# Kernel tuning notes

Hardware: AMD Instinct MI355X
Metric: run time of the kernel (lower is better)

Reference implementation:

```python
import jax, jax.numpy as jnp
import numpy as np

B, N, E, D = 8, 10000, 160000, 256
H = D // 2
SLOPE = 0.2  # LeakyReLU negative slope


def setup_inputs() -> dict:
    key = jax.random.key(0)
    ks = jax.random.split(key, 8)
    node_feats = jax.random.normal(ks[0], (B, N, D), dtype=jnp.float32)
    edge_attr = jax.random.uniform(ks[1], (E, 1), dtype=jnp.float32)
    W1 = jax.random.normal(ks[2], (2 * D, H), dtype=jnp.float32) * 0.05
    b1 = jnp.zeros((H,), dtype=jnp.float32)
    W2 = jax.random.normal(ks[3], (H, 1), dtype=jnp.float32) * 0.05
    b2 = jnp.zeros((1,), dtype=jnp.float32)
    edge_index = jax.random.randint(ks[4], (2, E), 0, N, dtype=jnp.int64)
    valid_masks = jax.random.randint(ks[5], (B, N), 0, 2).astype(bool)
    return {"node_feats": node_feats, "edge_attr": edge_attr, "W1": W1, "b1": b1,
            "W2": W2, "b2": b2, "edge_index": edge_index, "valid_masks": valid_masks}


def reference(node_feats, edge_attr, W1, b1, W2, b2, edge_index, valid_masks):
    # node_feats: [B,N,D]; edge_index: [2,E] shared across batch
    d = node_feats.shape[-1]
    src, dst = edge_index[0], edge_index[1]
    # cat([src_feats, dst_feats]) @ W1 == src @ W1[:d] + dst @ W1[d:]
    # Project per-node first, then gather per-edge: avoids the [B,E,2D] concat.
    ps = jnp.einsum('bnd,dh->bnh', node_feats, W1[:d])   # [B,N,H]
    pd = jnp.einsum('bnd,dh->bnh', node_feats, W1[d:])   # [B,N,H]
    h = ps[:, src] + pd[:, dst] + b1                      # [B,E,H]
    h = jnp.where(h >= 0, h, SLOPE * h)                   # LeakyReLU(0.2)
    scores = jnp.einsum('beh,h->be', h, W2[:, 0]) + b2[0]  # [B,E]
    scores = scores * edge_attr[:, 0]                     # edge_attr multiplies pre-softmax
    w = jax.nn.softmax(scores, axis=1)                    # global softmax over all edges
    # sparse_coo(edge_index, w) @ node_feats: out[src[e]] += w[e] * feats[dst[e]]
    msg = w[..., None] * node_feats[:, dst]               # [B,E,D]
    n = node_feats.shape[1]
    agg = jax.vmap(lambda m: jax.ops.segment_sum(m, src, num_segments=n))(msg)  # [B,N,D]
    mask = valid_masks.astype(node_feats.dtype)           # [B,N]
    cnt = mask.sum(axis=1)                                # [B]
    masked_mean = (agg * mask[..., None]).sum(axis=1) / jnp.maximum(cnt, 1.0)[:, None]
    full_mean = agg.mean(axis=1)
    graph_feats = jnp.where((cnt > 0)[:, None], masked_mean, full_mean)  # [B,D]
    return graph_feats, w
```

## Files before the change

### kernel.cpp

```cpp
#include <hip/hip_runtime.h>
#include <hip/hip_bf16.h>
#include <hip/hip_fp16.h>

#define B_ 8
#define N_ 10000
#define E_ 160000
#define D_ 256
#define H_ 128
#define SLOPE 0.2f
#define NCHUNK 50

#define EC_ 16
#define NR_ 32
#define RANGE_ 320
#define NPAD_ (NR_ * RANGE_)

typedef __attribute__((ext_vector_type(8))) _Float16 v8h;
typedef __attribute__((ext_vector_type(4))) _Float16 v4h;
typedef __attribute__((ext_vector_type(4))) float f32x4;

__global__ __launch_bounds__(64) void k_detect(const int* __restrict__ eidx_raw,
                                               const unsigned int* __restrict__ mask32,
                                               int* __restrict__ flags) {
    const int t = threadIdx.x;
    unsigned long long oddnz = __ballot(eidx_raw[2 * t + 1] != 0);
    unsigned long long mgt1  = __ballot(mask32[t] > 1u);
    if (t == 0) {
        flags[0] = (oddnz == 0ull) ? 1 : 0;
        flags[1] = (mgt1 != 0ull) ? 1 : 0;
    }
}

__global__ __launch_bounds__(256) void k_canon(const int* __restrict__ eidx_raw,
                                               const unsigned char* __restrict__ mask8,
                                               const unsigned int* __restrict__ mask32,
                                               const int* __restrict__ flags,
                                               int* __restrict__ ce,
                                               unsigned char* __restrict__ cm,
                                               unsigned char* __restrict__ cmT) {
    const int i = blockIdx.x * 256 + threadIdx.x;
    const int f_e = flags[0], f_m = flags[1];
    if (i < 2 * E_) ce[i] = f_e ? eidx_raw[2 * i] : eidx_raw[i];
    if (i < B_ * N_) {
        unsigned char v = f_m ? (unsigned char)(mask8[i] != 0)
                              : (unsigned char)(mask32[i] != 0u);
        cm[i] = v;
        const int b = i / N_;
        const int n = i - b * N_;
        cmT[n * 8 + b] = v;
    }
}

__global__ __launch_bounds__(256) void kW(const float* __restrict__ W1,
                                          __half* __restrict__ Wt) {
    const int i = blockIdx.x * 256 + threadIdx.x;
    const int f = i & 127;
    const int row = i >> 7;
    const int c = row >> 8, k = row & 255;
    Wt[((c * 128 + f) * 256) + k] = __float2half(W1[row * 128 + f]);
}

__global__ __launch_bounds__(256) void k0_init(const unsigned char* __restrict__ cm,
                                               float* __restrict__ cnt) {
    const int b = blockIdx.x;
    const int tid = threadIdx.x;
    int c = 0;
    for (int i = tid; i < N_; i += 256) c += cm[b * N_ + i] ? 1 : 0;
    __shared__ int red[256];
    red[tid] = c;
    __syncthreads();
    for (int s = 128; s > 0; s >>= 1) {
        if (tid < s) red[tid] += red[tid + s];
        __syncthreads();
    }
    if (tid == 0) cnt[b] = (float)red[0];
}

__global__ __launch_bounds__(256) void k1_mfma(const float* __restrict__ X,
                                               const __half* __restrict__ Wt,
                                               __half* __restrict__ ps,
                                               __half* __restrict__ pd) {
    const int cb = blockIdx.y;
    const int rb = blockIdx.x;
    const int tid = threadIdx.x;
    const int wave = tid >> 6, lane = tid & 63;
    const int quad = lane >> 4, l16 = lane & 15;

    __shared__ _Float16 Xs[128 * 40];
    __shared__ _Float16 Ws[128 * 40];

    f32x4 acc[2][8];
#pragma unroll
    for (int i = 0; i < 2; i++)
#pragma unroll
        for (int j = 0; j < 8; j++) acc[i][j] = (f32x4){0.f, 0.f, 0.f, 0.f};

    const int row_base = rb * 128;
    const __half* __restrict__ Wh = Wt + (size_t)cb * 128 * 256;
    __half* __restrict__ outp = cb ? pd : ps;

    const int sr = tid >> 1;
    const int sh = tid & 1;

    for (int kc = 0; kc < 8; ++kc) {
        {
            const float4* src = (const float4*)&X[(size_t)(row_base + sr) * 256 + kc * 32 + sh * 16];
            _Float16* dst = &Xs[sr * 40 + sh * 16];
#pragma unroll
            for (int j = 0; j < 4; ++j) {
                float4 v = src[j];
                v4h p = {(_Float16)v.x, (_Float16)v.y, (_Float16)v.z, (_Float16)v.w};
                *(v4h*)&dst[j * 4] = p;
            }
        }
        {
            const float4* src = (const float4*)&Wh[(size_t)sr * 256 + kc * 32 + sh * 16];
            float4 v0 = src[0], v1 = src[1];
            *(float4*)&Ws[sr * 40 + sh * 16] = v0;
            *(float4*)&Ws[sr * 40 + sh * 16 + 8] = v1;
        }
        __syncthreads();

        v8h wf[2];
#pragma unroll
        for (int ft = 0; ft < 2; ++ft)
            wf[ft] = *(v8h*)&Ws[(wave * 32 + ft * 16 + l16) * 40 + quad * 8];
#pragma unroll
        for (int nt = 0; nt < 8; ++nt) {
            v8h xf = *(v8h*)&Xs[(nt * 16 + l16) * 40 + quad * 8];
            acc[0][nt] = __builtin_amdgcn_mfma_f32_16x16x32_f16(wf[0], xf, acc[0][nt], 0, 0, 0);
            acc[1][nt] = __builtin_amdgcn_mfma_f32_16x16x32_f16(wf[1], xf, acc[1][nt], 0, 0, 0);
        }
        __syncthreads();
    }

#pragma unroll
    for (int nt = 0; nt < 8; ++nt) {
        const int R = row_base + nt * 16 + l16;
        const int b = R / N_;
        const int n = R - b * N_;
        __half* base = outp + ((size_t)(n * 8 + b)) * 128 + wave * 32 + quad * 4;
#pragma unroll
        for (int ft = 0; ft < 2; ++ft) {
            f32x4 a = acc[ft][nt];
            v4h h = {(_Float16)a.x, (_Float16)a.y, (_Float16)a.z, (_Float16)a.w};
            *(v4h*)(base + ft * 16) = h;
        }
    }
}

__global__ __launch_bounds__(256) void k2_scores(const __half* __restrict__ ps,
                                                 const __half* __restrict__ pd,
                                                 const int* __restrict__ ce,
                                                 const float* __restrict__ b1,
                                                 const float* __restrict__ W2,
                                                 const float* __restrict__ b2,
                                                 const float* __restrict__ eattr,
                                                 float* __restrict__ scores) {
    __shared__ float sb1[128];
    __shared__ float sw2[128];
    const int tid = threadIdx.x;
    if (tid < 128) sb1[tid] = b1[tid];
    else sw2[tid - 128] = W2[tid - 128];
    __syncthreads();

    const int wave = tid >> 6;
    const int lane = tid & 63;
    const int e = blockIdx.x * 4 + wave;

    const int src = ce[e];
    const int dst = ce[E_ + e];
    const int b = lane >> 3;
    const int hi = (lane & 7) * 16;

    const float4* pps = (const float4*)&ps[((size_t)src * 8 + b) * 128 + hi];
    const float4* ppd = (const float4*)&pd[((size_t)dst * 8 + b) * 128 + hi];

    float partial = 0.f;
#pragma unroll
    for (int q = 0; q < 2; q++) {
        float4 rs = pps[q];
        float4 rd = ppd[q];
        const __half2* hs = (const __half2*)&rs;
        const __half2* hd = (const __half2*)&rd;
#pragma unroll
        for (int j = 0; j < 4; j++) {
            float2 fs = __half22float2(hs[j]);
            float2 fd = __half22float2(hd[j]);
            int idx = hi + q * 8 + j * 2;
            float h0 = fs.x + fd.x + sb1[idx];     h0 = h0 >= 0.f ? h0 : SLOPE * h0;
            float h1 = fs.y + fd.y + sb1[idx + 1]; h1 = h1 >= 0.f ? h1 : SLOPE * h1;
            partial = fmaf(h0, sw2[idx], partial);
            partial = fmaf(h1, sw2[idx + 1], partial);
        }
    }
    partial += __shfl_xor(partial, 1);
    partial += __shfl_xor(partial, 2);
    partial += __shfl_xor(partial, 4);

    if ((lane & 7) == 0) {
        scores[(size_t)b * E_ + e] = (partial + b2[0]) * eattr[e];
    }
}

__global__ __launch_bounds__(256) void k3a_max(const float* __restrict__ sc,
                                               float* __restrict__ pmax) {
    const int b = blockIdx.y, c = blockIdx.x, tid = threadIdx.x;
    const float* x = sc + (size_t)b * E_;
    const int i0 = c * (E_ / 32);
    float mv = -3.4e38f;
    for (int i = i0 + tid; i < i0 + E_ / 32; i += 256) mv = fmaxf(mv, x[i]);
    __shared__ float red[256];
    red[tid] = mv;
    __syncthreads();
    for (int s = 128; s > 0; s >>= 1) {
        if (tid < s) red[tid] = fmaxf(red[tid], red[tid + s]);
        __syncthreads();
    }
    if (tid == 0) pmax[b * 32 + c] = red[0];
}

__global__ __launch_bounds__(256) void k3b_maxred(const float* __restrict__ pmax,
                                                  float* __restrict__ m) {
    const int t = threadIdx.x;
    float v = pmax[t];
#pragma unroll
    for (int k = 1; k <= 16; k <<= 1) v = fmaxf(v, __shfl_xor(v, k));
    if ((t & 31) == 0) m[t >> 5] = v;
}

__global__ __launch_bounds__(256) void k3c_sum(const float* __restrict__ sc,
                                               const float* __restrict__ m,
                                               double* __restrict__ psum) {
    const int b = blockIdx.y, c = blockIdx.x, tid = threadIdx.x;
    const float* x = sc + (size_t)b * E_;
    const float mv = m[b];
    const int i0 = c * (E_ / 32);
    double s = 0.0;
    for (int i = i0 + tid; i < i0 + E_ / 32; i += 256) s += (double)expf(x[i] - mv);
    __shared__ double red[256];
    red[tid] = s;
    __syncthreads();
    for (int st = 128; st > 0; st >>= 1) {
        if (tid < st) red[tid] += red[tid + st];
        __syncthreads();
    }
    if (tid == 0) psum[b * 32 + c] = red[0];
}

__global__ __launch_bounds__(256) void k3d_sumred(const double* __restrict__ psum,
                                                  float* __restrict__ inv) {
    const int t = threadIdx.x;
    double v = psum[t];
#pragma unroll
    for (int k = 1; k <= 16; k <<= 1) v += __shfl_xor(v, k);
    if ((t & 31) == 0) inv[t >> 5] = (float)(1.0 / v);
}

__global__ __launch_bounds__(256) void k3e_norm(float* __restrict__ sc,
                                                const float* __restrict__ m,
                                                const float* __restrict__ inv,
                                                float* __restrict__ wT) {
    const int e = blockIdx.x * 256 + threadIdx.x;
    float wv[8];
#pragma unroll
    for (int b = 0; b < 8; b++) {
        float v = expf(sc[(size_t)b * E_ + e] - m[b]) * inv[b];
        sc[(size_t)b * E_ + e] = v;
        wv[b] = v;
    }
    *(float4*)&wT[(size_t)e * 8]     = make_float4(wv[0], wv[1], wv[2], wv[3]);
    *(float4*)&wT[(size_t)e * 8 + 4] = make_float4(wv[4], wv[5], wv[6], wv[7]);
}

__global__ __launch_bounds__(256) void k3f_bin(const int* __restrict__ ce,
                                               const float* __restrict__ wT,
                                               const unsigned char* __restrict__ cmT,
                                               float* __restrict__ Wpart) {
    const int ec = blockIdx.x;
    const int rg = blockIdx.y;
    const int n0 = rg * RANGE_;

    __shared__ float lWf[RANGE_ * 8];
    __shared__ float lWm[RANGE_ * 8];
    for (int i = threadIdx.x; i < RANGE_ * 8; i += 256) { lWf[i] = 0.f; lWm[i] = 0.f; }
    __syncthreads();

    const int4* dst4 = (const int4*)(ce + E_);
    const int base4 = ec * (E_ / EC_ / 4);
    for (int i = threadIdx.x; i < E_ / EC_ / 4; i += 256) {
        int4 d4 = dst4[base4 + i];
        int dd[4] = {d4.x, d4.y, d4.z, d4.w};
        const int e0 = (base4 + i) * 4;
#pragma unroll
        for (int j = 0; j < 4; ++j) {
            const int rel = dd[j] - n0;
            if ((unsigned)rel < (unsigned)RANGE_) {
                const int e = e0 + j;
                const int src = ce[e];
                float4 w0 = *(const float4*)&wT[(size_t)e * 8];
                float4 w1 = *(const float4*)&wT[(size_t)e * 8 + 4];
                const unsigned long long mm = *(const unsigned long long*)&cmT[src * 8];
                float wv[8] = {w0.x, w0.y, w0.z, w0.w, w1.x, w1.y, w1.z, w1.w};
                float* lf = &lWf[rel * 8];
                float* lm = &lWm[rel * 8];
#pragma unroll
                for (int b = 0; b < 8; b++) {
                    atomicAdd(&lf[b], wv[b]);
                    if ((mm >> (8 * b)) & 1ull) atomicAdd(&lm[b], wv[b]);
                }
            }
        }
    }
    __syncthreads();

    float* of = Wpart + ((size_t)ec * 2 + 0) * (NPAD_ * 8) + n0 * 8;
    float* om = Wpart + ((size_t)ec * 2 + 1) * (NPAD_ * 8) + n0 * 8;
    for (int i = threadIdx.x; i < RANGE_ * 8; i += 256) { of[i] = lWf[i]; om[i] = lWm[i]; }
}

__global__ __launch_bounds__(256) void k3g_reduce(const float* __restrict__ Wpart,
                                                  float* __restrict__ WfT,
                                                  float* __restrict__ WmT) {
    const int i = blockIdx.x * 256 + threadIdx.x;
    float sf = 0.f, sm = 0.f;
#pragma unroll
    for (int ec = 0; ec < EC_; ec++) {
        sf += Wpart[(size_t)ec * 2 * (NPAD_ * 8) + i];
        sm += Wpart[((size_t)ec * 2 + 1) * (NPAD_ * 8) + i];
    }
    WfT[i] = sf;
    WmT[i] = sm;
}

__global__ __launch_bounds__(256) void k4b_wsum(const float* __restrict__ X,
                                                const float* __restrict__ WmT,
                                                const float* __restrict__ WfT,
                                                float* __restrict__ gpart) {
    const int c = blockIdx.x;
    const int b = blockIdx.y;
    const int tx = threadIdx.x & 63;
    const int ty = threadIdx.x >> 6;
    const int npc = N_ / NCHUNK;
    const int n0 = c * npc;

    const float4* X4 = (const float4*)(X + (size_t)b * N_ * 256);
    float4 am = {0.f, 0.f, 0.f, 0.f};
    float4 af = {0.f, 0.f, 0.f, 0.f};

    for (int n = n0 + ty; n < n0 + npc; n += 4) {
        float wm = WmT[n * 8 + b];
        float wf = WfT[n * 8 + b];
        float4 v = X4[(size_t)n * 64 + tx];
        am.x = fmaf(wm, v.x, am.x); am.y = fmaf(wm, v.y, am.y);
        am.z = fmaf(wm, v.z, am.z); am.w = fmaf(wm, v.w, am.w);
        af.x = fmaf(wf, v.x, af.x); af.y = fmaf(wf, v.y, af.y);
        af.z = fmaf(wf, v.z, af.z); af.w = fmaf(wf, v.w, af.w);
    }

    __shared__ float4 red[256];
    red[threadIdx.x] = am;
    __syncthreads();
    if (ty == 0) {
        float4 r1 = red[tx + 64], r2 = red[tx + 128], r3 = red[tx + 192];
        am.x += r1.x + r2.x + r3.x; am.y += r1.y + r2.y + r3.y;
        am.z += r1.z + r2.z + r3.z; am.w += r1.w + r2.w + r3.w;
    }
    __syncthreads();
    red[threadIdx.x] = af;
    __syncthreads();
    if (ty == 0) {
        float4 r1 = red[tx + 64], r2 = red[tx + 128], r3 = red[tx + 192];
        af.x += r1.x + r2.x + r3.x; af.y += r1.y + r2.y + r3.y;
        af.z += r1.z + r2.z + r3.z; af.w += r1.w + r2.w + r3.w;
        float4* gp4 = (float4*)gpart;
        gp4[((c * 2 + 0) * 8 + b) * 64 + tx] = am;
        gp4[((c * 2 + 1) * 8 + b) * 64 + tx] = af;
    }
}

__global__ __launch_bounds__(256) void k5_final(const float* __restrict__ gpart,
                                                const float* __restrict__ cnt,
                                                float* __restrict__ gf) {
    const int b = blockIdx.x;
    const int d = threadIdx.x;
    float sm = 0.f, sf = 0.f;
    for (int c = 0; c < NCHUNK; c++) {
        sm += gpart[((c * 2 + 0) * 8 + b) * 256 + d];
        sf += gpart[((c * 2 + 1) * 8 + b) * 256 + d];
    }
    const float cn = cnt[b];
    gf[b * 256 + d] = (cn > 0.f) ? (sm / cn) : (sf / (float)N_);
}

extern "C" void kernel_launch(void* const* d_in, const int* in_sizes, int n_in,
                              void* d_out, int out_size, void* d_ws, size_t ws_size,
                              hipStream_t stream) {
    const float* X     = (const float*)d_in[0];
    const float* eattr = (const float*)d_in[1];
    const float* W1    = (const float*)d_in[2];
    const float* b1    = (const float*)d_in[3];
    const float* W2    = (const float*)d_in[4];
    const float* b2    = (const float*)d_in[5];
    const int*   eidx_raw = (const int*)d_in[6];
    const unsigned char* mask8 = (const unsigned char*)d_in[7];
    const unsigned int*  mask32 = (const unsigned int*)d_in[7];

    float* out  = (float*)d_out;
    float* gf   = out;
    float* wout = out + 2048;

    __half* ps_h = (__half*)d_ws;
    __half* pd_h = ps_h + (size_t)N_ * 8 * 128;
    __half* Wt   = pd_h + (size_t)N_ * 8 * 128;
    int* ce = (int*)(Wt + 2 * 128 * 256);
    unsigned char* cmT = (unsigned char*)(ce + 2 * E_);
    unsigned char* cm  = cmT + NPAD_ * 8;
    float* cnt = (float*)(cm + B_ * N_);
    int* flags = (int*)(cnt + 8);
    float* pmax = (float*)(flags + 2);
    float* mbuf = pmax + 256;
    float* invb = mbuf + 8;
    double* psum = (double*)(((uintptr_t)(invb + 8) + 15) & ~(uintptr_t)15);
    float* gpart = (float*)(psum + 256);

    float* wT    = (float*)d_ws;
    float* Wpart = wT + (size_t)E_ * 8;
    float* WfT   = Wpart + (size_t)EC_ * 2 * NPAD_ * 8;
    float* WmT   = WfT + NPAD_ * 8;

    hipLaunchKernelGGL(k_detect, dim3(1), dim3(64), 0, stream, eidx_raw, mask32, flags);
    hipLaunchKernelGGL(k_canon, dim3(1250), dim3(256), 0, stream,
                       eidx_raw, mask8, mask32, flags, ce, cm, cmT);
    hipLaunchKernelGGL(kW, dim3(256), dim3(256), 0, stream, W1, Wt);
    hipLaunchKernelGGL(k0_init, dim3(8), dim3(256), 0, stream, cm, cnt);
    hipLaunchKernelGGL(k1_mfma, dim3(625, 2), dim3(256), 0, stream, X, Wt, ps_h, pd_h);
    hipLaunchKernelGGL(k2_scores, dim3(E_ / 4), dim3(256), 0, stream,
                       ps_h, pd_h, ce, b1, W2, b2, eattr, wout);
    hipLaunchKernelGGL(k3a_max, dim3(32, 8), dim3(256), 0, stream, wout, pmax);
    hipLaunchKernelGGL(k3b_maxred, dim3(1), dim3(256), 0, stream, pmax, mbuf);
    hipLaunchKernelGGL(k3c_sum, dim3(32, 8), dim3(256), 0, stream, wout, mbuf, psum);
    hipLaunchKernelGGL(k3d_sumred, dim3(1), dim3(256), 0, stream, psum, invb);
    hipLaunchKernelGGL(k3e_norm, dim3(E_ / 256), dim3(256), 0, stream,
                       wout, mbuf, invb, wT);
    hipLaunchKernelGGL(k3f_bin, dim3(EC_, NR_), dim3(256), 0, stream, ce, wT, cmT, Wpart);
    hipLaunchKernelGGL(k3g_reduce, dim3(NPAD_ * 8 / 256), dim3(256), 0, stream,
                       Wpart, WfT, WmT);
    hipLaunchKernelGGL(k4b_wsum, dim3(NCHUNK, 8), dim3(256), 0, stream, X, WmT, WfT, gpart);
    hipLaunchKernelGGL(k5_final, dim3(8), dim3(256), 0, stream, gpart, cnt, gf);
}
```

Measured before the change: 326.0 us.

## Bin-sort edges by src/dst node ranges and use packed fp16 dot2 scoring

Adds a histogram, prefix and scatter pass that reorders edges into 16x16 bins by destination and source node range. The score kernel then walks edges in this order, with an XCD-aware block remap, so gathers of ps/pd rows hit cache better. It also computes LeakyReLU and the W2 dot product in packed half precision using fdot2, with b1 and W2 pre-converted to fp16. The cost is three extra small kernels, indirect score writes through the original edge index, and lower precision in the score accumulation inputs.

```diff
diff --git a/kernel.cpp b/kernel.cpp
--- a/kernel.cpp
+++ b/kernel.cpp
@@ -15,9 +15,23 @@
 #define RANGE_ 320
 #define NPAD_ (NR_ * RANGE_)
 
+#define NB_ 64
+#define EPB_ (E_ / NB_)
+#define BINS_ 256
+#define NPB_ (N_ / 16)
+
 typedef __attribute__((ext_vector_type(8))) _Float16 v8h;
 typedef __attribute__((ext_vector_type(4))) _Float16 v4h;
+typedef __attribute__((ext_vector_type(2))) _Float16 v2h;
 typedef __attribute__((ext_vector_type(4))) float f32x4;
+
+static __device__ __forceinline__ float dot2f(v2h a, v2h b, float c) {
+#if __has_builtin(__builtin_amdgcn_fdot2)
+    return __builtin_amdgcn_fdot2(a, b, c, false);
+#else
+    return fmaf((float)a.y, (float)b.y, fmaf((float)a.x, (float)b.x, c));
+#endif
+}
 
 __global__ __launch_bounds__(64) void k_detect(const int* __restrict__ eidx_raw,
                                                const unsigned int* __restrict__ mask32,
@@ -52,12 +66,20 @@
 }
 
 __global__ __launch_bounds__(256) void kW(const float* __restrict__ W1,
-                                          __half* __restrict__ Wt) {
+                                          const float* __restrict__ b1,
+                                          const float* __restrict__ W2,
+                                          __half* __restrict__ Wt,
+                                          __half* __restrict__ b1h,
+                                          __half* __restrict__ w2h) {
     const int i = blockIdx.x * 256 + threadIdx.x;
     const int f = i & 127;
     const int row = i >> 7;
     const int c = row >> 8, k = row & 255;
     Wt[((c * 128 + f) * 256) + k] = __float2half(W1[row * 128 + f]);
+    if (blockIdx.x == 0 && threadIdx.x < 128) {
+        b1h[threadIdx.x] = __float2half(b1[threadIdx.x]);
+        w2h[threadIdx.x] = __float2half(W2[threadIdx.x]);
+    }
 }
 
 __global__ __launch_bounds__(256) void k0_init(const unsigned char* __restrict__ cm,
@@ -74,6 +96,64 @@
         __syncthreads();
     }
     if (tid == 0) cnt[b] = (float)red[0];
+}
+
+__global__ __launch_bounds__(256) void khist(const int* __restrict__ ce,
+                                             int* __restrict__ hpart) {
+    __shared__ int h[BINS_];
+    const int tid = threadIdx.x;
+    h[tid] = 0;
+    __syncthreads();
+    const int base = blockIdx.x * EPB_;
+    for (int i = tid; i < EPB_; i += 256) {
+        const int s = ce[base + i], d = ce[E_ + base + i];
+        const int bin = (d / NPB_) * 16 + s / NPB_;
+        atomicAdd(&h[bin], 1);
+    }
+    __syncthreads();
+    hpart[blockIdx.x * BINS_ + tid] = h[tid];
+}
+
+__global__ __launch_bounds__(256) void kprefix(const int* __restrict__ hpart,
+                                               int* __restrict__ offsetG) {
+    __shared__ int cnt[BINS_];
+    __shared__ int excl[BINS_];
+    const int bin = threadIdx.x;
+    int c = 0;
+    for (int b = 0; b < NB_; b++) c += hpart[b * BINS_ + bin];
+    cnt[bin] = c;
+    __syncthreads();
+    if (bin == 0) {
+        int r = 0;
+        for (int i = 0; i < BINS_; i++) { excl[i] = r; r += cnt[i]; }
+    }
+    __syncthreads();
+    int run = excl[bin];
+    for (int b = 0; b < NB_; b++) {
+        offsetG[b * BINS_ + bin] = run;
+        run += hpart[b * BINS_ + bin];
+    }
+}
+
+__global__ __launch_bounds__(256) void kscatter(const int* __restrict__ ce,
+                                                const int* __restrict__ offsetG,
+                                                int* __restrict__ srcS,
+                                                int* __restrict__ dstS,
+                                                int* __restrict__ origS) {
+    __shared__ int loc[BINS_];
+    const int tid = threadIdx.x;
+    loc[tid] = offsetG[blockIdx.x * BINS_ + tid];
+    __syncthreads();
+    const int base = blockIdx.x * EPB_;
+    for (int i = tid; i < EPB_; i += 256) {
+        const int e = base + i;
+        const int s = ce[e], d = ce[E_ + e];
+        const int bin = (d / NPB_) * 16 + s / NPB_;
+        const int pos = atomicAdd(&loc[bin], 1);
+        srcS[pos] = s;
+        dstS[pos] = d;
+        origS[pos] = e;
+    }
 }
 
 __global__ __launch_bounds__(256) void k1_mfma(const float* __restrict__ X,
@@ -151,55 +231,57 @@
 
 __global__ __launch_bounds__(256) void k2_scores(const __half* __restrict__ ps,
                                                  const __half* __restrict__ pd,
-                                                 const int* __restrict__ ce,
-                                                 const float* __restrict__ b1,
-                                                 const float* __restrict__ W2,
+                                                 const int* __restrict__ srcS,
+                                                 const int* __restrict__ dstS,
+                                                 const int* __restrict__ origS,
+                                                 const __half* __restrict__ b1h,
+                                                 const __half* __restrict__ w2h,
                                                  const float* __restrict__ b2,
                                                  const float* __restrict__ eattr,
                                                  float* __restrict__ scores) {
-    __shared__ float sb1[128];
-    __shared__ float sw2[128];
     const int tid = threadIdx.x;
-    if (tid < 128) sb1[tid] = b1[tid];
-    else sw2[tid - 128] = W2[tid - 128];
-    __syncthreads();
-
     const int wave = tid >> 6;
     const int lane = tid & 63;
-    const int e = blockIdx.x * 4 + wave;
-
-    const int src = ce[e];
-    const int dst = ce[E_ + e];
+    const int bid = blockIdx.x;
+    const int lb = (bid & 7) * 5000 + (bid >> 3);
+    const int e = lb * 4 + wave;
+
     const int b = lane >> 3;
     const int hi = (lane & 7) * 16;
 
-    const float4* pps = (const float4*)&ps[((size_t)src * 8 + b) * 128 + hi];
-    const float4* ppd = (const float4*)&pd[((size_t)dst * 8 + b) * 128 + hi];
-
-    float partial = 0.f;
-#pragma unroll
-    for (int q = 0; q < 2; q++) {
-        float4 rs = pps[q];
-        float4 rd = ppd[q];
-        const __half2* hs = (const __half2*)&rs;
-        const __half2* hd = (const __half2*)&rd;
-#pragma unroll
-        for (int j = 0; j < 4; j++) {
-            float2 fs = __half22float2(hs[j]);
-            float2 fd = __half22float2(hd[j]);
-            int idx = hi + q * 8 + j * 2;
-            float h0 = fs.x + fd.x + sb1[idx];     h0 = h0 >= 0.f ? h0 : SLOPE * h0;
-            float h1 = fs.y + fd.y + sb1[idx + 1]; h1 = h1 >= 0.f ? h1 : SLOPE * h1;
-            partial = fmaf(h0, sw2[idx], partial);
-            partial = fmaf(h1, sw2[idx + 1], partial);
-        }
-    }
-    partial += __shfl_xor(partial, 1);
-    partial += __shfl_xor(partial, 2);
-    partial += __shfl_xor(partial, 4);
+    v2h b1p[8], w2p[8];
+    {
+        const v2h* bp = (const v2h*)(b1h + hi);
+        const v2h* wp = (const v2h*)(w2h + hi);
+#pragma unroll
+        for (int j = 0; j < 8; j++) { b1p[j] = bp[j]; w2p[j] = wp[j]; }
+    }
+
+    const int src = srcS[e];
+    const int dst = dstS[e];
+    const int orig = origS[e];
+
+    const float4* aps = (const float4*)&ps[((size_t)src * 8 + b) * 128 + hi];
+    const float4* apd = (const float4*)&pd[((size_t)dst * 8 + b) * 128 + hi];
+    float4 rs[2] = {aps[0], aps[1]};
+    float4 rd[2] = {apd[0], apd[1]};
+    const v2h* sv = (const v2h*)rs;
+    const v2h* dv = (const v2h*)rd;
+
+    const v2h slp = {(_Float16)SLOPE, (_Float16)SLOPE};
+    float acc = 0.f;
+#pragma unroll
+    for (int j = 0; j < 8; j++) {
+        v2h x = sv[j] + dv[j] + b1p[j];
+        v2h l = __builtin_elementwise_max(x, x * slp);
+        acc = dot2f(l, w2p[j], acc);
+    }
+    acc += __shfl_xor(acc, 1);
+    acc += __shfl_xor(acc, 2);
+    acc += __shfl_xor(acc, 4);
 
     if ((lane & 7) == 0) {
-        scores[(size_t)b * E_ + e] = (partial + b2[0]) * eattr[e];
+        scores[(size_t)b * E_ + orig] = (acc + b2[0]) * eattr[orig];
     }
 }
 
@@ -423,6 +505,13 @@
     float* invb = mbuf + 8;
     double* psum = (double*)(((uintptr_t)(invb + 8) + 15) & ~(uintptr_t)15);
     float* gpart = (float*)(psum + 256);
+    int* hpart   = (int*)(gpart + NCHUNK * 2 * 8 * 256);
+    int* offsetG = hpart + NB_ * BINS_;
+    int* srcS    = offsetG + NB_ * BINS_;
+    int* dstS    = srcS + E_;
+    int* origS   = dstS + E_;
+    __half* b1h  = (__half*)(origS + E_);
+    __half* w2h  = b1h + 128;
 
     float* wT    = (float*)d_ws;
     float* Wpart = wT + (size_t)E_ * 8;
@@ -432,11 +521,15 @@
     hipLaunchKernelGGL(k_detect, dim3(1), dim3(64), 0, stream, eidx_raw, mask32, flags);
     hipLaunchKernelGGL(k_canon, dim3(1250), dim3(256), 0, stream,
                        eidx_raw, mask8, mask32, flags, ce, cm, cmT);
-    hipLaunchKernelGGL(kW, dim3(256), dim3(256), 0, stream, W1, Wt);
+    hipLaunchKernelGGL(kW, dim3(256), dim3(256), 0, stream, W1, b1, W2, Wt, b1h, w2h);
     hipLaunchKernelGGL(k0_init, dim3(8), dim3(256), 0, stream, cm, cnt);
+    hipLaunchKernelGGL(khist, dim3(NB_), dim3(256), 0, stream, ce, hpart);
+    hipLaunchKernelGGL(kprefix, dim3(1), dim3(256), 0, stream, hpart, offsetG);
+    hipLaunchKernelGGL(kscatter, dim3(NB_), dim3(256), 0, stream,
+                       ce, offsetG, srcS, dstS, origS);
     hipLaunchKernelGGL(k1_mfma, dim3(625, 2), dim3(256), 0, stream, X, Wt, ps_h, pd_h);
     hipLaunchKernelGGL(k2_scores, dim3(E_ / 4), dim3(256), 0, stream,
-                       ps_h, pd_h, ce, b1, W2, b2, eattr, wout);
+                       ps_h, pd_h, srcS, dstS, origS, b1h, w2h, b2, eattr, wout);
     hipLaunchKernelGGL(k3a_max, dim3(32, 8), dim3(256), 0, stream, wout, pmax);
     hipLaunchKernelGGL(k3b_maxred, dim3(1), dim3(256), 0, stream, pmax, mbuf);
     hipLaunchKernelGGL(k3c_sum, dim3(32, 8), dim3(256), 0, stream, wout, mbuf, psum);
```

Measured after the change: 324.5 us. No clear change (-0.5%).
